# Kernel optimization log

Hardware: AMD Instinct MI355X
Metric: run time of the kernel (lower is better)

## Reference

```python
import jax, jax.numpy as jnp
import numpy as np

N_NODES = 8192


def _gcn_norm(edge_index, num_nodes):
    # PyG GCNConv default: add self-loops, symmetric normalization.
    src, dst = edge_index[0], edge_index[1]
    loop = jnp.arange(num_nodes, dtype=src.dtype)
    src = jnp.concatenate([src, loop])
    dst = jnp.concatenate([dst, loop])
    deg = jax.ops.segment_sum(jnp.ones_like(dst, dtype=jnp.float32), dst,
                              num_segments=num_nodes)
    dis = jnp.where(deg > 0, jax.lax.rsqrt(jnp.maximum(deg, 1.0)), 0.0)
    norm = dis[src] * dis[dst]  # [E + N]
    return src, dst, norm


def _gcn_conv(x, W, b, src, dst, norm, num_nodes):
    h = x @ W                           # [N, F_out] dense GEMM
    msg = h[src] * norm[:, None]        # gather + scale, [E+N, F_out]
    out = jax.ops.segment_sum(msg, dst, num_segments=num_nodes)  # scatter-add
    return out + b


def setup_inputs() -> dict:
    key = jax.random.key(0)
    ks = jax.random.split(key, 8)
    N, E, F_in, H1, H2, F_out = N_NODES, 65536, 512, 4096, 1024, 10
    x = jax.random.normal(ks[0], (N, F_in), dtype=jnp.float32)
    edge_index = jax.random.randint(ks[1], (2, E), 0, N, dtype=jnp.int64)
    # Glorot-ish scaled weights
    W1 = jax.random.normal(ks[2], (F_in, H1), dtype=jnp.float32) * (1.0 / np.sqrt(F_in))
    b1 = jnp.zeros((H1,), dtype=jnp.float32)
    W2 = jax.random.normal(ks[3], (H1, H2), dtype=jnp.float32) * (1.0 / np.sqrt(H1))
    b2 = jnp.zeros((H2,), dtype=jnp.float32)
    W3 = jax.random.normal(ks[4], (H2, F_out), dtype=jnp.float32) * (1.0 / np.sqrt(H2))
    b3 = jnp.zeros((F_out,), dtype=jnp.float32)
    return {"x": x, "W1": W1, "b1": b1, "W2": W2, "b2": b2,
            "W3": W3, "b3": b3, "edge_index": edge_index}


def reference(x, W1, b1, W2, b2, W3, b3, edge_index):
    N = N_NODES
    src, dst, norm = _gcn_norm(edge_index, N)
    h = _gcn_conv(x.astype(jnp.float32), W1, b1, src, dst, norm, N)
    h = jax.nn.relu(h)  # dropout is identity in eval mode
    h = _gcn_conv(h, W2, b2, src, dst, norm, N)
    h = jax.nn.relu(h)
    h = _gcn_conv(h, W3, b3, src, dst, norm, N)
    return jax.nn.log_softmax(h, axis=1)
```

## Files before the change

### kernel.cpp

```cpp
#include <hip/hip_runtime.h>
#include <math.h>

#define N_NODES 8192
#define N_EDGES 65536
#define F_IN    512
#define HID1    4096
#define HID2    1024
#define F_OUT   10
#define H3_STRIDE 16
#define W3B_STRIDE 1032

typedef __bf16 bf16x8 __attribute__((ext_vector_type(8)));
typedef float floatx4 __attribute__((ext_vector_type(4)));
typedef float floatx16 __attribute__((ext_vector_type(16)));

static __device__ __forceinline__ unsigned short f2bf(float f) {
    union { float f; unsigned u; } v; v.f = f;
    unsigned r = v.u + 0x7fffu + ((v.u >> 16) & 1u);
    return (unsigned short)(r >> 16);
}
static __device__ __forceinline__ float bf2f(unsigned short u) {
    union { unsigned u; float f; } v; v.u = ((unsigned)u) << 16;
    return v.f;
}
static __device__ __forceinline__ void unpack8(uint4 r, float* f) {
    union { unsigned u; float v; } c;
    c.u = r.x << 16;          f[0] = c.v;
    c.u = r.x & 0xffff0000u;  f[1] = c.v;
    c.u = r.y << 16;          f[2] = c.v;
    c.u = r.y & 0xffff0000u;  f[3] = c.v;
    c.u = r.z << 16;          f[4] = c.v;
    c.u = r.z & 0xffff0000u;  f[5] = c.v;
    c.u = r.w << 16;          f[6] = c.v;
    c.u = r.w & 0xffff0000u;  f[7] = c.v;
}
static __device__ __forceinline__ uint4 pack8(const float* f) {
    uint4 o;
    o.x = (unsigned)f2bf(f[0]) | ((unsigned)f2bf(f[1]) << 16);
    o.y = (unsigned)f2bf(f[2]) | ((unsigned)f2bf(f[3]) << 16);
    o.z = (unsigned)f2bf(f[4]) | ((unsigned)f2bf(f[5]) << 16);
    o.w = (unsigned)f2bf(f[6]) | ((unsigned)f2bf(f[7]) << 16);
    return o;
}

__global__ __launch_bounds__(1024) void hist_scan_kernel(
        const int* __restrict__ ei, int* __restrict__ deg,
        int* __restrict__ row_ptr, int* __restrict__ cnt) {
    __shared__ int hist[N_NODES];
    __shared__ int sums[1024];
    int t = threadIdx.x;
#pragma unroll
    for (int i = 0; i < 8; i++) hist[t + i * 1024] = 0;
    __syncthreads();
    const int4* ei4 = (const int4*)(ei + N_EDGES);
#pragma unroll
    for (int i = 0; i < 16; i++) {
        int4 d4 = ei4[i * 1024 + t];
        atomicAdd(&hist[d4.x], 1);
        atomicAdd(&hist[d4.y], 1);
        atomicAdd(&hist[d4.z], 1);
        atomicAdd(&hist[d4.w], 1);
    }
    __syncthreads();
    int base = t * 8;
    int local[8], run = 0;
#pragma unroll
    for (int i = 0; i < 8; i++) {
        int dv = hist[base + i];
        deg[base + i] = dv;
        cnt[base + i] = 0;
        local[i] = run; run += dv;
    }
    sums[t] = run;
    __syncthreads();
    for (int off = 1; off < 1024; off <<= 1) {
        int val = (t >= off) ? sums[t - off] : 0;
        __syncthreads();
        sums[t] += val;
        __syncthreads();
    }
    int offset = (t == 0) ? 0 : sums[t - 1];
#pragma unroll
    for (int i = 0; i < 8; i++) row_ptr[base + i] = offset + local[i];
    if (t == 1023) row_ptr[N_NODES] = sums[1023];
}

static __device__ __forceinline__ void transpose_body(
        const float* __restrict__ W, unsigned short* __restrict__ Wt,
        int K, int N, int k0, int n0, int tid, float (*t)[33]) {
    int c = tid & 31, r8 = tid >> 5;
#pragma unroll
    for (int i = 0; i < 4; i++) {
        int r = r8 + i * 8;
        t[r][c] = W[(size_t)(k0 + r) * N + n0 + c];
    }
    __syncthreads();
#pragma unroll
    for (int i = 0; i < 4; i++) {
        int r = r8 + i * 8;
        Wt[(size_t)(n0 + r) * K + k0 + c] = f2bf(t[c][r]);
    }
}

__global__ __launch_bounds__(256) void megaprep_kernel(
        const int* __restrict__ ei, const int* __restrict__ deg,
        const int* __restrict__ row_ptr, int* __restrict__ cnt,
        int* __restrict__ csr_src, float* __restrict__ csr_w,
        const float* __restrict__ x, unsigned short* __restrict__ xb,
        const float* __restrict__ W1, unsigned short* __restrict__ W1t,
        const float* __restrict__ W2, unsigned short* __restrict__ W2t,
        const float* __restrict__ W3, unsigned short* __restrict__ w3b) {
    __shared__ float t[32][33];
    int b = blockIdx.x, tid = threadIdx.x;
    if (b < 256) {
        int e = b * 256 + tid;
        int s = ei[e];
        int d = ei[N_EDGES + e];
        int slot = row_ptr[d] + atomicAdd(&cnt[d], 1);
        csr_src[slot] = s;
        csr_w[slot] = rsqrtf((float)((deg[s] + 1) * (deg[d] + 1)));
    } else if (b < 4352) {
        int i = (b - 256) * 256 + tid;
        float4 a = ((const float4*)x)[i];
        ushort4 o;
        o.x = f2bf(a.x); o.y = f2bf(a.y); o.z = f2bf(a.z); o.w = f2bf(a.w);
        ((ushort4*)xb)[i] = o;
    } else if (b < 6400) {
        int bb = b - 4352;
        transpose_body(W1, W1t, F_IN, HID1, (bb >> 7) * 32, (bb & 127) * 32, tid, t);
    } else if (b < 10496) {
        int bb = b - 6400;
        transpose_body(W2, W2t, HID1, HID2, (bb >> 5) * 32, (bb & 31) * 32, tid, t);
    } else {
        for (int i = tid; i < HID2 * F_OUT; i += 256) {
            int k = i / F_OUT, c = i % F_OUT;
            w3b[c * W3B_STRIDE + k] = f2bf(W3[i]);
        }
    }
}

__global__ __launch_bounds__(256) void agg1_kernel(
        const unsigned short* __restrict__ xb, const int* __restrict__ row_ptr,
        const int* __restrict__ csr_src, const float* __restrict__ csr_w,
        const int* __restrict__ deg, unsigned short* __restrict__ out) {
    int v = blockIdx.x * 4 + (threadIdx.x >> 6);
    int t = threadIdx.x & 63;
    const uint4* xp = (const uint4*)xb;
    float sw = 1.0f / (float)(deg[v] + 1);
    float acc[8], tmp[8];
    unpack8(xp[(size_t)v * 64 + t], tmp);
#pragma unroll
    for (int j = 0; j < 8; j++) acc[j] = sw * tmp[j];
    int e = row_ptr[v], end = row_ptr[v + 1];
    for (; e + 4 <= end; e += 4) {
        int s0 = csr_src[e], s1 = csr_src[e + 1];
        int s2 = csr_src[e + 2], s3 = csr_src[e + 3];
        float w0 = csr_w[e], w1 = csr_w[e + 1];
        float w2 = csr_w[e + 2], w3 = csr_w[e + 3];
        float f0[8], f1[8], f2[8], f3[8];
        unpack8(xp[(size_t)s0 * 64 + t], f0);
        unpack8(xp[(size_t)s1 * 64 + t], f1);
        unpack8(xp[(size_t)s2 * 64 + t], f2);
        unpack8(xp[(size_t)s3 * 64 + t], f3);
#pragma unroll
        for (int j = 0; j < 8; j++)
            acc[j] += w0 * f0[j] + w1 * f1[j] + w2 * f2[j] + w3 * f3[j];
    }
    for (; e < end; e++) {
        int s = csr_src[e];
        float w = csr_w[e];
        float f0[8];
        unpack8(xp[(size_t)s * 64 + t], f0);
#pragma unroll
        for (int j = 0; j < 8; j++) acc[j] += w * f0[j];
    }
    ((uint4*)out)[(size_t)v * 64 + t] = pack8(acc);
}

__global__ __launch_bounds__(256) void agg2_gemm3_kernel(
        const unsigned short* __restrict__ h, const int* __restrict__ row_ptr,
        const int* __restrict__ csr_src, const float* __restrict__ csr_w,
        const int* __restrict__ deg, const float* __restrict__ b2,
        const unsigned short* __restrict__ w3b, float* __restrict__ H3) {
    __shared__ unsigned short w3s[F_OUT * W3B_STRIDE];
    __shared__ float red[4][F_OUT];
    int tid = threadIdx.x;
    for (int i = tid; i < F_OUT * W3B_STRIDE; i += 256) w3s[i] = w3b[i];
    __syncthreads();
    int half = tid >> 7;
    int t = tid & 127;
    int v = blockIdx.x * 2 + half;
    const uint4* hp = (const uint4*)h;
    float sw = 1.0f / (float)(deg[v] + 1);
    float acc[8], tmp[8];
    unpack8(hp[(size_t)v * 128 + t], tmp);
#pragma unroll
    for (int j = 0; j < 8; j++) acc[j] = sw * tmp[j];
    int e = row_ptr[v], end = row_ptr[v + 1];
    for (; e + 4 <= end; e += 4) {
        int s0 = csr_src[e], s1 = csr_src[e + 1];
        int s2 = csr_src[e + 2], s3 = csr_src[e + 3];
        float w0 = csr_w[e], w1 = csr_w[e + 1];
        float w2 = csr_w[e + 2], w3 = csr_w[e + 3];
        float f0[8], f1[8], f2[8], f3[8];
        unpack8(hp[(size_t)s0 * 128 + t], f0);
        unpack8(hp[(size_t)s1 * 128 + t], f1);
        unpack8(hp[(size_t)s2 * 128 + t], f2);
        unpack8(hp[(size_t)s3 * 128 + t], f3);
#pragma unroll
        for (int j = 0; j < 8; j++)
            acc[j] += w0 * f0[j] + w1 * f1[j] + w2 * f2[j] + w3 * f3[j];
    }
    for (; e < end; e++) {
        int s = csr_src[e];
        float w = csr_w[e];
        float f0[8];
        unpack8(hp[(size_t)s * 128 + t], f0);
#pragma unroll
        for (int j = 0; j < 8; j++) acc[j] += w * f0[j];
    }
    float4 b4a = ((const float4*)b2)[t * 2];
    float4 b4b = ((const float4*)b2)[t * 2 + 1];
    acc[0] = fmaxf(acc[0] + b4a.x, 0.0f); acc[1] = fmaxf(acc[1] + b4a.y, 0.0f);
    acc[2] = fmaxf(acc[2] + b4a.z, 0.0f); acc[3] = fmaxf(acc[3] + b4a.w, 0.0f);
    acc[4] = fmaxf(acc[4] + b4b.x, 0.0f); acc[5] = fmaxf(acc[5] + b4b.y, 0.0f);
    acc[6] = fmaxf(acc[6] + b4b.z, 0.0f); acc[7] = fmaxf(acc[7] + b4b.w, 0.0f);

    float partial[F_OUT];
#pragma unroll
    for (int c = 0; c < F_OUT; c++) {
        float wf[8];
        unpack8(*(const uint4*)&w3s[c * W3B_STRIDE + t * 8], wf);
        partial[c] = acc[0] * wf[0] + acc[1] * wf[1] + acc[2] * wf[2] + acc[3] * wf[3]
                   + acc[4] * wf[4] + acc[5] * wf[5] + acc[6] * wf[6] + acc[7] * wf[7];
    }
#pragma unroll
    for (int c = 0; c < F_OUT; c++) {
#pragma unroll
        for (int off = 32; off > 0; off >>= 1)
            partial[c] += __shfl_xor(partial[c], off, 64);
    }
    int wave = tid >> 6, lane = tid & 63;
    if (lane == 0) {
#pragma unroll
        for (int c = 0; c < F_OUT; c++) red[wave][c] = partial[c];
    }
    __syncthreads();
    if (tid < 2 * F_OUT) {
        int hh = tid / F_OUT, c = tid % F_OUT;
        H3[(size_t)(blockIdx.x * 2 + hh) * H3_STRIDE + c] =
            red[hh * 2][c] + red[hh * 2 + 1][c];
    }
}

#define P8_STAGE(mat_, kh_, dd_, base_, k0_) do {                              \
    unsigned short* L_ = lds + ((dd_) * 4 + (mat_) * 2 + (kh_)) * 8192;        \
    _Pragma("unroll")                                                          \
    for (int j = 0; j < 2; j++) {                                              \
        int slot = j * 512 + tid;                                              \
        int s4 = slot >> 4, cs = slot & 15;                                    \
        int csp = cs ^ (s4 & 3);                                               \
        int grow = s4 * 4 + (csp >> 2);                                        \
        int gcol = (csp & 3) * 8;                                              \
        __builtin_amdgcn_global_load_lds(                                      \
            (const __attribute__((address_space(1))) void*)((base_) + (size_t)grow * K + (k0_) + (kh_) * 32 + gcol), \
            (__attribute__((address_space(3))) void*)(&L_[slot * 8]), 16, 0, 0); \
    }                                                                          \
} while (0)

#define P8_OFF(R_, lc_) ((((R_) >> 2) * 128) + (((((R_) & 3) << 2) | (lc_)) ^ (((R_) >> 2) & 3)) * 8)

#define P8_MAIN_LOOP(NT_)                                                      \
    P8_STAGE(0, 0, 0, Abase, 0);                                               \
    P8_STAGE(1, 0, 0, Bbase, 0);                                               \
    P8_STAGE(0, 1, 0, Abase, 0);                                               \
    P8_STAGE(1, 1, 0, Bbase, 0);                                               \
    asm volatile("s_waitcnt vmcnt(4)" ::: "memory");                           \
    __builtin_amdgcn_s_barrier();                                              \
    for (int t = 0; t < (NT_); t++) {                                          \
        int d = t & 1, dn = d ^ 1;                                             \
        int k1 = (t + 1) * 64;                                                 \
        _Pragma("unroll")                                                      \
        for (int kk = 0; kk < 4; kk++) {                                       \
            if (kk == 2) {                                                     \
                if (t + 1 < (NT_))                                             \
                    asm volatile("s_waitcnt vmcnt(4)" ::: "memory");           \
                else                                                           \
                    asm volatile("s_waitcnt vmcnt(0)" ::: "memory");           \
                __builtin_amdgcn_s_barrier();                                  \
            }                                                                  \
            int kh = kk >> 1;                                                  \
            int lc0 = (kk & 1) * 2 + lhalf;                                    \
            const unsigned short* Ak = lds + (d * 4 + kh) * 8192;              \
            const unsigned short* Bk = lds + (d * 4 + 2 + kh) * 8192;          \
            bf16x8 af[4], bfr[2];                                              \
            _Pragma("unroll")                                                  \
            for (int mt = 0; mt < 4; mt++) {                                   \
                int R = wm * 128 + mt * 32 + lrow;                             \
                af[mt] = *(const bf16x8*)&Ak[P8_OFF(R, lc0)];                  \
            }                                                                  \
            _Pragma("unroll")                                                  \
            for (int nt = 0; nt < 2; nt++) {                                   \
                int R = wn * 64 + nt * 32 + lrow;                              \
                bfr[nt] = *(const bf16x8*)&Bk[P8_OFF(R, lc0)];                 \
            }                                                                  \
            if (t + 1 < (NT_)) {                                               \
                if (kk == 0)      P8_STAGE(0, 0, dn, Abase, k1);               \
                else if (kk == 1) P8_STAGE(1, 0, dn, Bbase, k1);               \
                else if (kk == 2) P8_STAGE(0, 1, dn, Abase, k1);               \
                else              P8_STAGE(1, 1, dn, Bbase, k1);               \
            }                                                                  \
            __builtin_amdgcn_s_barrier();                                      \
            __builtin_amdgcn_s_setprio(1);                                     \
            _Pragma("unroll")                                                  \
            for (int mt = 0; mt < 4; mt++)                                     \
                _Pragma("unroll")                                              \
                for (int nt = 0; nt < 2; nt++)                                 \
                    acc[mt][nt] = __builtin_amdgcn_mfma_f32_32x32x16_bf16(     \
                        af[mt], bfr[nt], acc[mt][nt], 0, 0, 0);                \
            __builtin_amdgcn_s_setprio(0);                                     \
            if (kk == 0 || kk == 2) __builtin_amdgcn_s_barrier();              \
        }                                                                      \
        asm volatile("s_waitcnt vmcnt(4)" ::: "memory");                       \
        __builtin_amdgcn_s_barrier();                                          \
    }

__global__ __launch_bounds__(512, 2) void gemm1_pipe8_kernel(
        const unsigned short* __restrict__ A,
        const unsigned short* __restrict__ Bt,
        const float* __restrict__ bias,
        unsigned short* __restrict__ C) {
    __shared__ unsigned short lds[65536];
    const int K = F_IN, N = HID1;
    int tid = threadIdx.x;
    int wave = tid >> 6, lane = tid & 63;
    int wm = wave >> 2, wn = wave & 3;
    int lrow = lane & 31, lhalf = lane >> 5;

    int b = blockIdx.x;
    int GN = HID1 >> 8;
    int ntile = (b >> 3) % GN;
    int mtile = ((b >> 3) / GN) * 8 + (b & 7);
    int m0 = mtile * 256, n0 = ntile * 256;

    const unsigned short* Abase = A + (size_t)m0 * K;
    const unsigned short* Bbase = Bt + (size_t)n0 * K;

    floatx16 acc[4][2] = {};
    P8_MAIN_LOOP(8)

#pragma unroll
    for (int mt = 0; mt < 4; mt++) {
#pragma unroll
        for (int nt = 0; nt < 2; nt++) {
            int col = n0 + wn * 64 + nt * 32 + lrow;
            float bv = bias[col];
#pragma unroll
            for (int reg = 0; reg < 16; reg++) {
                int row = m0 + wm * 128 + mt * 32 + (reg & 3) + 8 * (reg >> 2) + 4 * lhalf;
                float v = fmaxf(acc[mt][nt][reg] + bv, 0.0f);
                C[(size_t)row * N + col] = f2bf(v);
            }
        }
    }
}

__global__ __launch_bounds__(512, 2) void gemm2_pipe8_split_kernel(
        const unsigned short* __restrict__ A,
        const unsigned short* __restrict__ Bt,
        unsigned short* __restrict__ Ca,
        unsigned short* __restrict__ Cb) {
    __shared__ unsigned short lds[65536];
    const int K = HID1;
    const int N = HID2;
    int tid = threadIdx.x;
    int wave = tid >> 6, lane = tid & 63;
    int wm = wave >> 2, wn = wave & 3;
    int lrow = lane & 31, lhalf = lane >> 5;

    int b = blockIdx.x;
    int u = b >> 3;
    int col = u & 7;
    int mtile = (u >> 3) * 8 + (b & 7);
    int ntile = col >> 1;
    int ksp = col & 1;
    int m0 = mtile * 256, n0 = ntile * 256;
    int koff = ksp * (HID1 / 2);

    const unsigned short* Abase = A + (size_t)m0 * K + koff;
    const unsigned short* Bbase = Bt + (size_t)n0 * K + koff;
    unsigned short* Cout = ksp ? Cb : Ca;

    floatx16 acc[4][2] = {};
    P8_MAIN_LOOP(32)

#pragma unroll
    for (int mt = 0; mt < 4; mt++) {
#pragma unroll
        for (int nt = 0; nt < 2; nt++) {
            int colc = n0 + wn * 64 + nt * 32 + lrow;
#pragma unroll
            for (int reg = 0; reg < 16; reg++) {
                int row = m0 + wm * 128 + mt * 32 + (reg & 3) + 8 * (reg >> 2) + 4 * lhalf;
                Cout[(size_t)row * N + colc] = f2bf(acc[mt][nt][reg]);
            }
        }
    }
}

__global__ __launch_bounds__(256) void merge_kernel(
        const unsigned short* __restrict__ Ca, unsigned short* __restrict__ Cb) {
    const uint4* a4 = (const uint4*)Ca;
    uint4* b4 = (uint4*)Cb;
    int base = blockIdx.x * 1024 + threadIdx.x;
#pragma unroll
    for (int j = 0; j < 4; j++) {
        int i = base + j * 256;
        float fa[8], fb[8];
        unpack8(a4[i], fa);
        unpack8(b4[i], fb);
#pragma unroll
        for (int k = 0; k < 8; k++) fa[k] += fb[k];
        b4[i] = pack8(fa);
    }
}

__global__ void final_kernel(const float* __restrict__ h3, const int* __restrict__ row_ptr,
                             const int* __restrict__ csr_src, const float* __restrict__ csr_w,
                             const int* __restrict__ deg, const float* __restrict__ b3,
                             float* __restrict__ out) {
    int v = blockIdx.x * blockDim.x + threadIdx.x;
    if (v >= N_NODES) return;
    const float4* h4 = (const float4*)h3;
    float sw = 1.0f / (float)(deg[v] + 1);
    float a[12];
    *(float4*)&a[0] = h4[v * 4];
    *(float4*)&a[4] = h4[v * 4 + 1];
    *(float4*)&a[8] = h4[v * 4 + 2];
    float acc[F_OUT];
#pragma unroll
    for (int c = 0; c < F_OUT; c++) acc[c] = b3[c] + sw * a[c];
    int end = row_ptr[v + 1];
    for (int e = row_ptr[v]; e < end; e++) {
        int s = csr_src[e];
        float w = csr_w[e];
        float bsrc[12];
        *(float4*)&bsrc[0] = h4[s * 4];
        *(float4*)&bsrc[4] = h4[s * 4 + 1];
        *(float4*)&bsrc[8] = h4[s * 4 + 2];
#pragma unroll
        for (int c = 0; c < F_OUT; c++) acc[c] += w * bsrc[c];
    }
    float m = acc[0];
#pragma unroll
    for (int c = 1; c < F_OUT; c++) m = fmaxf(m, acc[c]);
    float ssum = 0.0f;
#pragma unroll
    for (int c = 0; c < F_OUT; c++) ssum += expf(acc[c] - m);
    float l = logf(ssum);
#pragma unroll
    for (int c = 0; c < F_OUT; c++) out[v * F_OUT + c] = acc[c] - m - l;
}

extern "C" void kernel_launch(void* const* d_in, const int* in_sizes, int n_in,
                              void* d_out, int out_size, void* d_ws, size_t ws_size,
                              hipStream_t stream) {
    const float* x  = (const float*)d_in[0];
    const float* W1 = (const float*)d_in[1];
    const float* b1 = (const float*)d_in[2];
    const float* W2 = (const float*)d_in[3];
    const float* b2 = (const float*)d_in[4];
    const float* W3 = (const float*)d_in[5];
    const float* b3 = (const float*)d_in[6];
    const int*   ei = (const int*)d_in[7];
    float* out = (float*)d_out;

    char* p = (char*)d_ws;
    int*   deg     = (int*)p;    p += N_NODES * 4;
    int*   cnt     = (int*)p;    p += N_NODES * 4;
    int*   row_ptr = (int*)p;    p += 33024;
    int*   csr_src = (int*)p;    p += N_EDGES * 4;
    float* csr_w   = (float*)p;  p += N_EDGES * 4;
    float* h3      = (float*)p;  p += N_NODES * H3_STRIDE * 4;
    unsigned short* w3b = (unsigned short*)p; p += (F_OUT * W3B_STRIDE * 2 + 255) / 256 * 256;
    unsigned short* xb    = (unsigned short*)p; p += (size_t)N_NODES * F_IN * 2;
    unsigned short* agg_x = (unsigned short*)p; p += (size_t)N_NODES * F_IN * 2;
    unsigned short* W1t   = (unsigned short*)p; p += (size_t)HID1 * F_IN * 2;
    unsigned short* W2t   = (unsigned short*)p; p += (size_t)HID2 * HID1 * 2;
    unsigned short* h1    = (unsigned short*)p; p += (size_t)N_NODES * HID1 * 2;
    unsigned short* h2pre = (unsigned short*)p; p += (size_t)N_NODES * HID2 * 2;
    unsigned short* h2a = xb;

    hist_scan_kernel<<<1, 1024, 0, stream>>>(ei, deg, row_ptr, cnt);
    megaprep_kernel<<<10497, 256, 0, stream>>>(ei, deg, row_ptr, cnt, csr_src, csr_w,
                                               x, xb, W1, W1t, W2, W2t, W3, w3b);

    agg1_kernel<<<N_NODES / 4, 256, 0, stream>>>(xb, row_ptr, csr_src, csr_w, deg, agg_x);
    gemm1_pipe8_kernel<<<(N_NODES / 256) * (HID1 / 256), 512, 0, stream>>>(
        agg_x, W1t, b1, h1);

    gemm2_pipe8_split_kernel<<<256, 512, 0, stream>>>(h1, W2t, h2a, h2pre);
    merge_kernel<<<1024, 256, 0, stream>>>(h2a, h2pre);

    agg2_gemm3_kernel<<<N_NODES / 2, 256, 0, stream>>>(h2pre, row_ptr, csr_src, csr_w,
                                                       deg, b2, w3b, h3);

    final_kernel<<<N_NODES / 256, 256, 0, stream>>>(h3, row_ptr, csr_src, csr_w, deg, b3, out);
}
```

Measured before the change: 274.6 us.

## Use 4-stage LDS pipeline in GEMM2 and parallelize degree histogram

The split-K GEMM2 kernel moves from a double-buffered 64-wide K pipeline to a four-buffer ring of 32-wide K stages, prefetching three stages ahead and issuing the loads interleaved with the MFMA steps. The goal is to hide global-to-LDS latency better and lower barrier stalls. Separately, the single-block histogram+scan becomes a memset, a grid-wide atomic histogram and a single-block scan, which removes the serialized one-block histogram at the cost of two extra launches and global atomics.

```diff
diff --git a/kernel.cpp b/kernel.cpp
--- a/kernel.cpp
+++ b/kernel.cpp
@@ -43,35 +43,27 @@
     return o;
 }
 
-__global__ __launch_bounds__(1024) void hist_scan_kernel(
-        const int* __restrict__ ei, int* __restrict__ deg,
-        int* __restrict__ row_ptr, int* __restrict__ cnt) {
-    __shared__ int hist[N_NODES];
+__global__ __launch_bounds__(256) void hist_kernel(
+        const int* __restrict__ ei, int* __restrict__ deg) {
+    int e = blockIdx.x * 256 + threadIdx.x;
+    atomicAdd(&deg[ei[N_EDGES + e]], 1);
+}
+
+__global__ __launch_bounds__(1024) void scan_kernel(
+        const int* __restrict__ deg, int* __restrict__ row_ptr,
+        int* __restrict__ cnt) {
     __shared__ int sums[1024];
     int t = threadIdx.x;
-#pragma unroll
-    for (int i = 0; i < 8; i++) hist[t + i * 1024] = 0;
-    __syncthreads();
-    const int4* ei4 = (const int4*)(ei + N_EDGES);
-#pragma unroll
-    for (int i = 0; i < 16; i++) {
-        int4 d4 = ei4[i * 1024 + t];
-        atomicAdd(&hist[d4.x], 1);
-        atomicAdd(&hist[d4.y], 1);
-        atomicAdd(&hist[d4.z], 1);
-        atomicAdd(&hist[d4.w], 1);
-    }
-    __syncthreads();
     int base = t * 8;
+    int4 d0 = ((const int4*)deg)[t * 2];
+    int4 d1 = ((const int4*)deg)[t * 2 + 1];
+    int dv[8] = {d0.x, d0.y, d0.z, d0.w, d1.x, d1.y, d1.z, d1.w};
     int local[8], run = 0;
 #pragma unroll
-    for (int i = 0; i < 8; i++) {
-        int dv = hist[base + i];
-        deg[base + i] = dv;
-        cnt[base + i] = 0;
-        local[i] = run; run += dv;
-    }
+    for (int i = 0; i < 8; i++) { local[i] = run; run += dv[i]; }
     sums[t] = run;
+    ((int4*)cnt)[t * 2] = make_int4(0, 0, 0, 0);
+    ((int4*)cnt)[t * 2 + 1] = make_int4(0, 0, 0, 0);
     __syncthreads();
     for (int off = 1; off < 1024; off <<= 1) {
         int val = (t >= off) ? sums[t - off] : 0;
@@ -253,22 +245,25 @@
     }
 }
 
-#define P8_STAGE(mat_, kh_, dd_, base_, k0_) do {                              \
-    unsigned short* L_ = lds + ((dd_) * 4 + (mat_) * 2 + (kh_)) * 8192;        \
+#define P8_OFF(R_, lc_) ((((R_) >> 2) * 128) + (((((R_) & 3) << 2) | (lc_)) ^ (((R_) >> 2) & 3)) * 8)
+
+#define Q4_STAGE(Lbuf_, base_, k0_) do {                                       \
+    unsigned short* L_ = (Lbuf_);                                              \
     _Pragma("unroll")                                                          \
     for (int j = 0; j < 2; j++) {                                              \
-        int slot = j * 512 + tid;                                              \
-        int s4 = slot >> 4, cs = slot & 15;                                    \
+        int sl = j * 512 + tid;                                                \
+        int s4 = sl >> 4, cs = sl & 15;                                        \
         int csp = cs ^ (s4 & 3);                                               \
         int grow = s4 * 4 + (csp >> 2);                                        \
         int gcol = (csp & 3) * 8;                                              \
         __builtin_amdgcn_global_load_lds(                                      \
-            (const __attribute__((address_space(1))) void*)((base_) + (size_t)grow * K + (k0_) + (kh_) * 32 + gcol), \
-            (__attribute__((address_space(3))) void*)(&L_[slot * 8]), 16, 0, 0); \
+            (const __attribute__((address_space(1))) void*)((base_) + (size_t)grow * K + (k0_) + gcol), \
+            (__attribute__((address_space(3))) void*)(&L_[sl * 8]), 16, 0, 0); \
     }                                                                          \
 } while (0)
 
-#define P8_OFF(R_, lc_) ((((R_) >> 2) * 128) + (((((R_) & 3) << 2) | (lc_)) ^ (((R_) >> 2) & 3)) * 8)
+#define P8_STAGE(mat_, kh_, dd_, base_, k0_) \
+    Q4_STAGE(lds + ((dd_) * 4 + (mat_) * 2 + (kh_)) * 8192, base_, (k0_) + (kh_) * 32)
 
 #define P8_MAIN_LOOP(NT_)                                                      \
     P8_STAGE(0, 0, 0, Abase, 0);                                               \
@@ -365,7 +360,7 @@
     }
 }
 
-__global__ __launch_bounds__(512, 2) void gemm2_pipe8_split_kernel(
+__global__ __launch_bounds__(512, 2) void gemm2_q4_split_kernel(
         const unsigned short* __restrict__ A,
         const unsigned short* __restrict__ Bt,
         unsigned short* __restrict__ Ca,
@@ -392,7 +387,54 @@
     unsigned short* Cout = ksp ? Cb : Ca;
 
     floatx16 acc[4][2] = {};
-    P8_MAIN_LOOP(32)
+    const int NT = (HID1 / 2) >> 5;
+
+    Q4_STAGE(lds + 0 * 16384, Abase, 0);  Q4_STAGE(lds + 0 * 16384 + 8192, Bbase, 0);
+    Q4_STAGE(lds + 1 * 16384, Abase, 32); Q4_STAGE(lds + 1 * 16384 + 8192, Bbase, 32);
+    Q4_STAGE(lds + 2 * 16384, Abase, 64); Q4_STAGE(lds + 2 * 16384 + 8192, Bbase, 64);
+    asm volatile("s_waitcnt vmcnt(8)" ::: "memory");
+    __builtin_amdgcn_s_barrier();
+
+    for (int t = 0; t < NT; t++) {
+        const unsigned short* Ak = lds + (size_t)(t & 3) * 16384;
+        const unsigned short* Bk = Ak + 8192;
+        unsigned short* Lnext = lds + (size_t)((t + 3) & 3) * 16384;
+        int k3 = (t + 3) * 32;
+#pragma unroll
+        for (int kk = 0; kk < 2; kk++) {
+            int lc0 = kk * 2 + lhalf;
+            bf16x8 af[4], bfr[2];
+#pragma unroll
+            for (int mt = 0; mt < 4; mt++) {
+                int R = wm * 128 + mt * 32 + lrow;
+                af[mt] = *(const bf16x8*)&Ak[P8_OFF(R, lc0)];
+            }
+#pragma unroll
+            for (int nt = 0; nt < 2; nt++) {
+                int R = wn * 64 + nt * 32 + lrow;
+                bfr[nt] = *(const bf16x8*)&Bk[P8_OFF(R, lc0)];
+            }
+            if (t + 3 < NT) {
+                if (kk == 0) Q4_STAGE(Lnext, Abase, k3);
+                else         Q4_STAGE(Lnext + 8192, Bbase, k3);
+            }
+            __builtin_amdgcn_s_setprio(1);
+#pragma unroll
+            for (int mt = 0; mt < 4; mt++)
+#pragma unroll
+                for (int nt = 0; nt < 2; nt++)
+                    acc[mt][nt] = __builtin_amdgcn_mfma_f32_32x32x16_bf16(
+                        af[mt], bfr[nt], acc[mt][nt], 0, 0, 0);
+            __builtin_amdgcn_s_setprio(0);
+        }
+        if (t + 3 < NT)
+            asm volatile("s_waitcnt vmcnt(8)" ::: "memory");
+        else if (t + 2 < NT)
+            asm volatile("s_waitcnt vmcnt(4)" ::: "memory");
+        else if (t + 1 < NT)
+            asm volatile("s_waitcnt vmcnt(0)" ::: "memory");
+        __builtin_amdgcn_s_barrier();
+    }
 
 #pragma unroll
     for (int mt = 0; mt < 4; mt++) {
@@ -491,7 +533,9 @@
     unsigned short* h2pre = (unsigned short*)p; p += (size_t)N_NODES * HID2 * 2;
     unsigned short* h2a = xb;
 
-    hist_scan_kernel<<<1, 1024, 0, stream>>>(ei, deg, row_ptr, cnt);
+    hipMemsetAsync(deg, 0, N_NODES * sizeof(int), stream);
+    hist_kernel<<<N_EDGES / 256, 256, 0, stream>>>(ei, deg);
+    scan_kernel<<<1, 1024, 0, stream>>>(deg, row_ptr, cnt);
     megaprep_kernel<<<10497, 256, 0, stream>>>(ei, deg, row_ptr, cnt, csr_src, csr_w,
                                                x, xb, W1, W1t, W2, W2t, W3, w3b);
 
@@ -499,7 +543,7 @@
     gemm1_pipe8_kernel<<<(N_NODES / 256) * (HID1 / 256), 512, 0, stream>>>(
         agg_x, W1t, b1, h1);
 
-    gemm2_pipe8_split_kernel<<<256, 512, 0, stream>>>(h1, W2t, h2a, h2pre);
+    gemm2_q4_split_kernel<<<256, 512, 0, stream>>>(h1, W2t, h2a, h2pre);
     merge_kernel<<<1024, 256, 0, stream>>>(h2a, h2pre);
 
     agg2_gemm3_kernel<<<N_NODES / 2, 256, 0, stream>>>(h2pre, row_ptr, csr_src, csr_w,
```

Result: slower. 289.8 us (+5.5%).
